# Performance work log

Measured on AMD Instinct MI355X. Metric: run time of the kernel, lower is better.

## Reference

```python
import jax, jax.numpy as jnp
import numpy as np

B, S, H, V, L = 8, 1024, 1024, 512, 6
NEG_INF = -10000000.0  # matches torch neg_inf constant


def setup_inputs() -> dict:
    key = jax.random.key(0)
    ks = jax.random.split(key, 13)
    s = 0.02
    return {
        "inputs": jax.random.randint(ks[0], (B, S), 0, V),
        "embedding": jax.random.normal(ks[1], (V, H), jnp.float32) * s,
        "Wq": jax.random.normal(ks[2], (L, H, H), jnp.float32) * s,
        "bq": jnp.zeros((L, H), jnp.float32),
        "Wk": jax.random.normal(ks[3], (L, H, H), jnp.float32) * s,
        "bk": jnp.zeros((L, H), jnp.float32),
        "Wv": jax.random.normal(ks[4], (L, H, H), jnp.float32) * s,
        "bv": jnp.zeros((L, H), jnp.float32),
        "Wm": jax.random.normal(ks[5], (L, H, H), jnp.float32) * s,
        "bm": jnp.zeros((L, H), jnp.float32),
        "Wout": jax.random.normal(ks[6], (H, V), jnp.float32) * s,
        "bout": jnp.zeros((V,), jnp.float32),
    }


def reference(inputs, embedding, Wq, bq, Wk, bk, Wv, bv, Wm, bm, Wout, bout):
    Hd = embedding.shape[1]
    seq = inputs.shape[1]
    scale = jax.lax.rsqrt(jnp.asarray(Hd, jnp.float32))
    idx = jnp.arange(seq)
    # mask[key, query]: additive NEG_INF where key > query (strict lower triangle)
    mask = jnp.where(idx[:, None] > idx[None, :], jnp.float32(NEG_INF), jnp.float32(0.0))
    x = embedding[inputs]  # [B, S, H]
    n_layers = Wq.shape[0]
    attns = []
    for l in range(n_layers):
        q = x @ Wq[l] + bq[l]
        k = x @ Wk[l] + bk[l]
        v = x @ Wv[l] + bv[l]
        # [B, key, query], softmax over key axis (dim=1), exactly as original
        logits = jnp.einsum('bkh,bqh->bkq', k, q) * scale + mask
        attn = jax.nn.softmax(logits, axis=1)
        ctx = jnp.einsum('bkq,bkh->bqh', attn, v)  # attn^T @ v
        residual = x + ctx
        x = residual + jax.nn.relu(ctx @ Wm[l] + bm[l])
        attns.append(attn)
    out = x @ Wout + bout  # [B, S, V]
    return out, jnp.stack(attns)  # attns: [L, B, S, S]
```

## Files before the change

### kernel.cpp

```cpp
#include <hip/hip_runtime.h>
#include <stdint.h>

typedef unsigned short u16;
typedef unsigned int u32;
typedef __bf16 bf16x8 __attribute__((ext_vector_type(8)));
typedef float floatx4 __attribute__((ext_vector_type(4)));

#define NEG_INF_F (-10000000.0f)

__device__ __forceinline__ float bf2f(u16 u) {
    union { u32 u; float f; } x; x.u = ((u32)u) << 16; return x.f;
}
__device__ __forceinline__ u16 f2bf(float f) {
    union { float f; u32 u; } x; x.f = f;
    u32 r = x.u + 0x7fffu + ((x.u >> 16) & 1u);
    return (u16)(r >> 16);
}

__device__ __forceinline__ void async_cp16(const void* g, void* l) {
    __builtin_amdgcn_global_load_lds(
        (const __attribute__((address_space(1))) void*)g,
        (__attribute__((address_space(3))) void*)l, 16, 0, 0);
}

enum { EPI_QKV = 0, EPI_LOGITS = 1, EPI_CTX = 2, EPI_MLP = 3, EPI_OUT = 4 };

template <int EPI>
__global__ __launch_bounds__(256) void gemm_bt(
    const u16* __restrict__ A, int lda, long long aBatch,
    const u16* __restrict__ B, int ldb, long long bBatch,
    void* __restrict__ Cv, int ldc, long long cBatch,
    int K,
    const float* __restrict__ bias,
    const u16* __restrict__ ctxb,
    u16* __restrict__ xb,
    float scale, int nx, int ny)
{
    __shared__ __align__(16) u16 sA[128 * 64];
    __shared__ __align__(16) u16 sB[128 * 64];

    const int tid  = threadIdx.x;
    const int wave = tid >> 6;
    const int lane = tid & 63;

    int bxE, byE, bz;
    if constexpr (EPI == EPI_LOGITS) {
        bz = blockIdx.x & 7;
        int t = blockIdx.x >> 3;
        int tq = (int)((sqrtf(8.0f * t + 1.0f) - 1.0f) * 0.5f);
        while ((tq + 1) * (tq + 2) / 2 <= t) ++tq;
        while (tq * (tq + 1) / 2 > t) --tq;
        bxE = tq;
        byE = t - tq * (tq + 1) / 2;
    } else if constexpr (EPI == EPI_CTX) {
        bz = blockIdx.x & 7;
        int t = blockIdx.x >> 3;
        bxE = t & 7;
        byE = t >> 3;
    } else {
        bz = 0;
        const int k = blockIdx.x & 7, r = blockIdx.x >> 3;
        if (nx >= 8) { const int xp = nx >> 3; bxE = xp * k + (r % xp); byE = r / xp; }
        else         { bxE = k >> 1; byE = (k & 1) * (ny >> 1) + r; }
    }
    int Keff = K;
    if constexpr (EPI == EPI_CTX) Keff = min(K, (byE + 1) * 128);

    const u16* Ab = A + (long long)bz * aBatch + (long long)(byE * 128) * lda;
    const u16* Bb = B + (long long)bz * bBatch + (long long)(bxE * 128) * ldb;

    const int wm = wave >> 1, wn = wave & 1;
    const int quad = lane >> 4;

    const int srowoff = lane >> 3;
    const int gf      = (lane & 7) ^ ((lane >> 3) & 7);

    const int ra = 64 * wm + (lane & 15);
    const int rb = 64 * wn + (lane & 15);
    const int rx7 = lane & 7;

    floatx4 zero = {0.f, 0.f, 0.f, 0.f};
    floatx4 acc[4][4];
#pragma unroll
    for (int i = 0; i < 4; ++i)
#pragma unroll
        for (int j = 0; j < 4; ++j) acc[i][j] = zero;

    for (int k0 = 0; k0 < Keff; k0 += 64) {
#pragma unroll
        for (int i = 0; i < 4; ++i) {
            const int c = wave * 4 + i;
            const int r = c * 8 + srowoff;
            async_cp16(Ab + (long long)r * lda + k0 + gf * 8, &sA[c * 512 + lane * 8]);
            async_cp16(Bb + (long long)r * ldb + k0 + gf * 8, &sB[c * 512 + lane * 8]);
        }
        __syncthreads();

#pragma unroll
        for (int kk = 0; kk < 64; kk += 32) {
            const int gbase = kk >> 3;
            const int ga = ((gbase + quad) ^ rx7) << 3;
            bf16x8 af[4], bf[4];
#pragma unroll
            for (int mi = 0; mi < 4; ++mi)
                af[mi] = *(const bf16x8*)&sA[(ra + 16 * mi) * 64 + ga];
#pragma unroll
            for (int ni = 0; ni < 4; ++ni)
                bf[ni] = *(const bf16x8*)&sB[(rb + 16 * ni) * 64 + ga];
#pragma unroll
            for (int mi = 0; mi < 4; ++mi)
#pragma unroll
                for (int ni = 0; ni < 4; ++ni)
                    acc[mi][ni] = __builtin_amdgcn_mfma_f32_16x16x32_bf16(
                        af[mi], bf[ni], acc[mi][ni], 0, 0, 0);
        }
        __syncthreads();
    }

    const int m0 = byE * 128 + 64 * wm + (quad << 2);
    const int n0 = bxE * 128 + 64 * wn + (lane & 15);
#pragma unroll
    for (int mi = 0; mi < 4; ++mi) {
#pragma unroll
        for (int ni = 0; ni < 4; ++ni) {
            const int gn = n0 + ni * 16;
#pragma unroll
            for (int r = 0; r < 4; ++r) {
                const int gm = m0 + mi * 16 + r;
                float v = acc[mi][ni][r];
                if constexpr (EPI == EPI_QKV) {
                    v += bias[gn];
                    ((u16*)Cv)[(long long)gm * ldc + gn] = f2bf(v);
                } else if constexpr (EPI == EPI_LOGITS) {
                    v = v * scale + (gm > gn ? NEG_INF_F : 0.0f);
                    ((float*)Cv)[(long long)bz * cBatch + (long long)gm * ldc + gn] = v;
                } else if constexpr (EPI == EPI_CTX) {
                    ((u16*)Cv)[(long long)bz * cBatch + (long long)gm * ldc + gn] = f2bf(v);
                } else if constexpr (EPI == EPI_MLP) {
                    const long long idx = (long long)gm * ldc + gn;
                    v += bias[gn];
                    v = fmaxf(v, 0.0f);
                    float xv = bf2f(xb[idx]) + bf2f(ctxb[idx]) + v;
                    xb[idx] = f2bf(xv);
                } else {
                    v += bias[gn];
                    ((float*)Cv)[(long long)gm * ldc + gn] = v;
                }
            }
        }
    }
}

template <int L, int H, int V>
__global__ void setup_weights(const float* __restrict__ Wq, const float* __restrict__ Wk,
                              const float* __restrict__ Wv, const float* __restrict__ Wm,
                              const float* __restrict__ Wout,
                              const float* __restrict__ bq, const float* __restrict__ bk,
                              const float* __restrict__ bv,
                              u16* __restrict__ WqkvT, u16* __restrict__ WmT,
                              u16* __restrict__ WoutT, float* __restrict__ bqkv)
{
    const int z = blockIdx.z;
    if (z == 4 * L + 1) {
        int i = ((blockIdx.y * 16 + blockIdx.x) * 256) + threadIdx.y * 64 + threadIdx.x;
        if (i < L * 3 * H) {
            int l = i / (3 * H), j = i % (3 * H);
            float v = (j < H) ? bq[l * H + j]
                    : (j < 2 * H) ? bk[l * H + j - H]
                                  : bv[l * H + j - 2 * H];
            bqkv[i] = v;
        }
        return;
    }

    const float* in;
    u16* outp;
    int inStride, outStride;
    if (z == 4 * L) {
        if (blockIdx.x >= V / 64) return;
        in = Wout; inStride = V;
        outp = WoutT; outStride = H;
    } else {
        const int which = z / L, l = z % L;
        inStride = H; outStride = H;
        if (which == 3) { in = Wm + (long long)l * H * H; outp = WmT + (long long)l * H * H; }
        else {
            in   = (which == 0 ? Wq : which == 1 ? Wk : Wv) + (long long)l * H * H;
            outp = WqkvT + (long long)l * 3 * H * H + (long long)which * H * H;
        }
    }

    __shared__ float tile[64][65];
    const int r0 = blockIdx.y * 64, c0 = blockIdx.x * 64;
    const int x = threadIdx.x, y = threadIdx.y;
#pragma unroll
    for (int j = 0; j < 16; ++j) {
        int r = y + j * 4;
        tile[r][x] = in[(long long)(r0 + r) * inStride + c0 + x];
    }
    __syncthreads();
#pragma unroll
    for (int j = 0; j < 16; ++j) {
        int r = y + j * 4;
        outp[(long long)(c0 + r) * outStride + r0 + x] = f2bf(tile[x][r]);
    }
}

__global__ __launch_bounds__(1024) void attn_post(
    float* __restrict__ attn, long long aStride,
    u16* __restrict__ attnT, long long tStride,
    const u16* __restrict__ qkv, u16* __restrict__ Vt)
{
    const int zone = blockIdx.y;
    if (zone < 8) {
        __shared__ float sm[64][16], sl[64][16], sm2[8][16], sl2[8][16];
        __shared__ float sM[16], sInv[16];

        float* base = attn + (long long)zone * aStride;
        const int x = threadIdx.x, ky = threadIdx.y;
        const int q = blockIdx.x * 16 + x;

        float v[16];
        float m = -3.4e38f, l = 0.f;
#pragma unroll
        for (int j = 0; j < 16; ++j) {
            const int k = ky * 16 + j;
            float vj = NEG_INF_F;
            if (k <= q) vj = base[(long long)k * 1024 + q];
            v[j] = vj;
            float mn = fmaxf(m, vj);
            l = l * __expf(m - mn) + __expf(vj - mn);
            m = mn;
        }
        sm[ky][x] = m;
        sl[ky][x] = l;
        __syncthreads();
        if (ky < 8) {
            float M = -3.4e38f, L = 0.f;
#pragma unroll
            for (int t = 0; t < 8; ++t) {
                float mm = sm[ky + 8 * t][x], ll = sl[ky + 8 * t][x];
                float mn = fmaxf(M, mm);
                L = L * __expf(M - mn) + ll * __expf(mm - mn);
                M = mn;
            }
            sm2[ky][x] = M;
            sl2[ky][x] = L;
        }
        __syncthreads();
        if (ky == 0) {
            float M = -3.4e38f, L = 0.f;
#pragma unroll
            for (int t = 0; t < 8; ++t) {
                float mm = sm2[t][x], ll = sl2[t][x];
                float mn = fmaxf(M, mm);
                L = L * __expf(M - mn) + ll * __expf(mm - mn);
                M = mn;
            }
            sM[x]   = M;
            sInv[x] = 1.0f / L;
        }
        __syncthreads();
        const float M = sM[x], inv = sInv[x];

        u16 pb[16];
#pragma unroll
        for (int j = 0; j < 16; ++j) {
            float p = __expf(v[j] - M) * inv;
            base[(long long)(ky * 16 + j) * 1024 + q] = p;
            pb[j] = f2bf(p);
        }
        u16* trow = attnT + (long long)zone * tStride + (long long)q * 1024 + ky * 16;
        ((uint4*)trow)[0] = *(const uint4*)&pb[0];
        ((uint4*)trow)[1] = *(const uint4*)&pb[8];
    } else {
        const int b = zone - 8;
        const u16* Vb = qkv + 2 * 1024 + (long long)b * (1024LL * 3072);
        u16* Ob       = Vt + (long long)b * (1024LL * 1024);
        __shared__ float tile[64][65];
        const int tid = threadIdx.y * 16 + threadIdx.x;
        const int tx = tid & 63, ty = tid >> 6;
#pragma unroll
        for (int rep = 0; rep < 4; ++rep) {
            const int T = blockIdx.x + rep * 64;
            const int s0 = (T >> 4) * 64, h0 = (T & 15) * 64;
            __syncthreads();
#pragma unroll
            for (int j = 0; j < 4; ++j) {
                const int s = j * 16 + ty;
                tile[s][tx] = bf2f(Vb[(long long)(s0 + s) * 3072 + h0 + tx]);
            }
            __syncthreads();
#pragma unroll
            for (int j = 0; j < 4; ++j) {
                const int h = j * 16 + ty;
                Ob[(long long)(h0 + h) * 1024 + s0 + tx] = f2bf(tile[tx][h]);
            }
        }
    }
}

__global__ void embed_kernel(const int* __restrict__ tok, const float* __restrict__ emb,
                             u16* __restrict__ xb)
{
    const int row = blockIdx.x;
    const int t   = tok[row];
    float4 v = ((const float4*)(emb + (long long)t * 1024))[threadIdx.x];
    uint2 p;
    p.x = (u32)f2bf(v.x) | ((u32)f2bf(v.y) << 16);
    p.y = (u32)f2bf(v.z) | ((u32)f2bf(v.w) << 16);
    ((uint2*)(xb + (long long)row * 1024))[threadIdx.x] = p;
}

extern "C" void kernel_launch(void* const* d_in, const int* in_sizes, int n_in,
                              void* d_out, int out_size, void* d_ws, size_t ws_size,
                              hipStream_t stream)
{
    const int*   tok  = (const int*)d_in[0];
    const float* emb  = (const float*)d_in[1];
    const float* Wq   = (const float*)d_in[2];
    const float* bq   = (const float*)d_in[3];
    const float* Wk   = (const float*)d_in[4];
    const float* bk   = (const float*)d_in[5];
    const float* Wv   = (const float*)d_in[6];
    const float* bv   = (const float*)d_in[7];
    const float* Wm   = (const float*)d_in[8];
    const float* bm   = (const float*)d_in[9];
    const float* Wout = (const float*)d_in[10];
    const float* bout = (const float*)d_in[11];
    float* out = (float*)d_out;

    constexpr int B = 8, S = 1024, H = 1024, V = 512, L = 6;
    constexpr long long M = (long long)B * S;

    char* ws = (char*)d_ws;
    u16*   WqkvT = (u16*)ws;   ws += (long long)L * 3 * H * H * 2;
    u16*   WmT   = (u16*)ws;   ws += (long long)L * H * H * 2;
    u16*   WoutT = (u16*)ws;   ws += (long long)V * H * 2;
    float* bqkv  = (float*)ws; ws += (long long)L * 3 * H * 4;
    u16*   xb    = (u16*)ws;   ws += M * H * 2;
    u16*   QKV   = (u16*)ws;   ws += M * 3 * H * 2;
    u16*   attnT = (u16*)ws;   ws += (long long)B * S * S * 2;
    u16*   Vt    = (u16*)ws;   ws += (long long)B * S * S * 2;
    u16*   ctxb  = (u16*)ws;   ws += M * H * 2;

    float* attnOut = out + (long long)B * S * V;

    setup_weights<L, H, V><<<dim3(16, 16, 4 * L + 2), dim3(64, 4), 0, stream>>>(
        Wq, Wk, Wv, Wm, Wout, bq, bk, bv, WqkvT, WmT, WoutT, bqkv);
    embed_kernel<<<M, 256, 0, stream>>>(tok, emb, xb);

    for (int l = 0; l < L; ++l) {
        gemm_bt<EPI_QKV><<<1536, 256, 0, stream>>>(
            xb, H, 0, WqkvT + (long long)l * 3 * H * H, H, 0,
            QKV, 3 * H, 0, H, bqkv + l * 3 * H, nullptr, nullptr, 0.f, 24, 64);

        float* attnL = attnOut + (long long)l * B * S * S;
        gemm_bt<EPI_LOGITS><<<288, 256, 0, stream>>>(
            QKV + H, 3 * H, (long long)S * 3 * H,
            QKV, 3 * H, (long long)S * 3 * H,
            attnL, S, (long long)S * S, H,
            nullptr, nullptr, nullptr, 0.03125f, 0, 0);

        attn_post<<<dim3(64, 16), dim3(16, 64), 0, stream>>>(
            attnL, (long long)S * S, attnT, (long long)S * S, QKV, Vt);

        gemm_bt<EPI_CTX><<<512, 256, 0, stream>>>(
            attnT, S, (long long)S * S, Vt, S, (long long)S * S,
            ctxb, H, (long long)S * H, S,
            nullptr, nullptr, nullptr, 0.f, 0, 0);

        gemm_bt<EPI_MLP><<<512, 256, 0, stream>>>(
            ctxb, H, 0, WmT + (long long)l * H * H, H, 0,
            nullptr, H, 0, H, bm + l * H, ctxb, xb, 0.f, 8, 64);
    }

    gemm_bt<EPI_OUT><<<256, 256, 0, stream>>>(
        xb, H, 0, WoutT, H, 0, out, V, 0, H,
        bout, nullptr, nullptr, 0.f, 4, 64);
}
```

Before: 1.357 ms.

## Add triple-buffered 256x128 GEMM kernel for QKV and MLP projections

Result: slower. 1.546 ms (+13.9%).

```diff
diff --git a/kernel.cpp b/kernel.cpp
--- a/kernel.cpp
+++ b/kernel.cpp
@@ -7,6 +7,7 @@
 typedef float floatx4 __attribute__((ext_vector_type(4)));
 
 #define NEG_INF_F (-10000000.0f)
+#define MFMA16 __builtin_amdgcn_mfma_f32_16x16x32_bf16
 
 __device__ __forceinline__ float bf2f(u16 u) {
     union { u32 u; float f; } x; x.u = ((u32)u) << 16; return x.f;
@@ -111,8 +112,7 @@
             for (int mi = 0; mi < 4; ++mi)
 #pragma unroll
                 for (int ni = 0; ni < 4; ++ni)
-                    acc[mi][ni] = __builtin_amdgcn_mfma_f32_16x16x32_bf16(
-                        af[mi], bf[ni], acc[mi][ni], 0, 0, 0);
+                    acc[mi][ni] = MFMA16(af[mi], bf[ni], acc[mi][ni], 0, 0, 0);
         }
         __syncthreads();
     }
@@ -151,6 +151,167 @@
     }
 }
 
+template <int EPI>
+__global__ __launch_bounds__(512, 2) void gemm3s(
+    const u16* __restrict__ A, int lda,
+    const u16* __restrict__ Bw, int ldb,
+    void* __restrict__ Cv, int ldc,
+    int K, const float* __restrict__ bias,
+    const u16* __restrict__ ctxb, u16* __restrict__ xb)
+{
+    __shared__ __align__(16) u16 sA[3][256 * 64];
+    __shared__ __align__(16) u16 sB[3][128 * 64];
+
+    const int tid  = threadIdx.x;
+    const int wave = tid >> 6;
+    const int lane = tid & 63;
+    const int wm   = wave >> 1, wn = wave & 1;
+    const int quad = lane >> 4;
+
+    const int k8 = blockIdx.x & 7;
+    const int r  = blockIdx.x >> 3;
+    const int bxE = r >> 2;
+    const int byE = k8 * 4 + (r & 3);
+
+    const u16* Ab = A  + (long long)(byE * 256) * lda;
+    const u16* Bb = Bw + (long long)(bxE * 128) * ldb;
+
+    const int srow = tid >> 3;
+    const int gf   = (tid & 7) ^ ((tid >> 3) & 7);
+    const long long aSrc = (long long)srow * lda + gf * 8;
+    const long long bSrc = (long long)srow * ldb + gf * 8;
+    const int dst = (wave << 9) + lane * 8;
+
+#define STA(nb, c, k0) async_cp16(Ab + (long long)((c) * 64) * lda + (k0) + aSrc, \
+                                  &sA[nb][(c) * 4096 + dst])
+#define STB(nb, c, k0) async_cp16(Bb + (long long)((c) * 64) * ldb + (k0) + bSrc, \
+                                  &sB[nb][(c) * 4096 + dst])
+
+    const int ra  = wm * 64 + (lane & 15);
+    const int rb  = wn * 64 + (lane & 15);
+    const int rx7 = lane & 7;
+
+    floatx4 zero = {0.f, 0.f, 0.f, 0.f};
+    floatx4 acc[4][4];
+#pragma unroll
+    for (int i = 0; i < 4; ++i)
+#pragma unroll
+        for (int j = 0; j < 4; ++j) acc[i][j] = zero;
+
+    const int NT = K >> 6;
+
+    STA(0, 0, 0);  STA(0, 1, 0);  STA(0, 2, 0);  STA(0, 3, 0);
+    STB(0, 0, 0);  STB(0, 1, 0);
+    STA(1, 0, 64); STA(1, 1, 64); STA(1, 2, 64); STA(1, 3, 64);
+    STB(1, 0, 64); STB(1, 1, 64);
+
+    int cb = 0;
+#pragma unroll 3
+    for (int t = 0; t < NT; ++t) {
+        if (t + 1 < NT) asm volatile("s_waitcnt vmcnt(6)" ::: "memory");
+        else            asm volatile("s_waitcnt vmcnt(0)" ::: "memory");
+        __builtin_amdgcn_s_barrier();
+
+        const int  nb = (cb == 0) ? 2 : cb - 1;
+        const int  kn = (t + 2) << 6;
+        const bool st = (t + 2) < NT;
+        const u16* pA = &sA[cb][0];
+        const u16* pB = &sB[cb][0];
+
+        bf16x8 af[4], bf0, bf1;
+
+        if (st) { STA(nb, 0, kn); STA(nb, 1, kn); }
+        {
+            const int g = (quad ^ rx7) << 3;
+#pragma unroll
+            for (int mi = 0; mi < 4; ++mi)
+                af[mi] = *(const bf16x8*)&pA[(ra + 16 * mi) * 64 + g];
+            bf0 = *(const bf16x8*)&pB[rb * 64 + g];
+            bf1 = *(const bf16x8*)&pB[(rb + 16) * 64 + g];
+        }
+        __builtin_amdgcn_s_setprio(1);
+#pragma unroll
+        for (int mi = 0; mi < 4; ++mi) {
+            acc[mi][0] = MFMA16(af[mi], bf0, acc[mi][0], 0, 0, 0);
+            acc[mi][1] = MFMA16(af[mi], bf1, acc[mi][1], 0, 0, 0);
+        }
+        __builtin_amdgcn_s_setprio(0);
+
+        if (st) { STA(nb, 2, kn); STA(nb, 3, kn); }
+        {
+            const int g = (quad ^ rx7) << 3;
+            bf0 = *(const bf16x8*)&pB[(rb + 32) * 64 + g];
+            bf1 = *(const bf16x8*)&pB[(rb + 48) * 64 + g];
+        }
+        __builtin_amdgcn_s_setprio(1);
+#pragma unroll
+        for (int mi = 0; mi < 4; ++mi) {
+            acc[mi][2] = MFMA16(af[mi], bf0, acc[mi][2], 0, 0, 0);
+            acc[mi][3] = MFMA16(af[mi], bf1, acc[mi][3], 0, 0, 0);
+        }
+        __builtin_amdgcn_s_setprio(0);
+
+        if (st) { STB(nb, 0, kn); }
+        {
+            const int g = ((4 + quad) ^ rx7) << 3;
+#pragma unroll
+            for (int mi = 0; mi < 4; ++mi)
+                af[mi] = *(const bf16x8*)&pA[(ra + 16 * mi) * 64 + g];
+            bf0 = *(const bf16x8*)&pB[rb * 64 + g];
+            bf1 = *(const bf16x8*)&pB[(rb + 16) * 64 + g];
+        }
+        __builtin_amdgcn_s_setprio(1);
+#pragma unroll
+        for (int mi = 0; mi < 4; ++mi) {
+            acc[mi][0] = MFMA16(af[mi], bf0, acc[mi][0], 0, 0, 0);
+            acc[mi][1] = MFMA16(af[mi], bf1, acc[mi][1], 0, 0, 0);
+        }
+        __builtin_amdgcn_s_setprio(0);
+
+        if (st) { STB(nb, 1, kn); }
+        {
+            const int g = ((4 + quad) ^ rx7) << 3;
+            bf0 = *(const bf16x8*)&pB[(rb + 32) * 64 + g];
+            bf1 = *(const bf16x8*)&pB[(rb + 48) * 64 + g];
+        }
+        __builtin_amdgcn_s_setprio(1);
+#pragma unroll
+        for (int mi = 0; mi < 4; ++mi) {
+            acc[mi][2] = MFMA16(af[mi], bf0, acc[mi][2], 0, 0, 0);
+            acc[mi][3] = MFMA16(af[mi], bf1, acc[mi][3], 0, 0, 0);
+        }
+        __builtin_amdgcn_s_setprio(0);
+
+        cb = (cb == 2) ? 0 : cb + 1;
+    }
+#undef STA
+#undef STB
+
+    const int m0 = byE * 256 + wm * 64 + (quad << 2);
+    const int n0 = bxE * 128 + wn * 64 + (lane & 15);
+#pragma unroll
+    for (int mi = 0; mi < 4; ++mi) {
+#pragma unroll
+        for (int ni = 0; ni < 4; ++ni) {
+            const int gn = n0 + ni * 16;
+            const float bb = bias[gn];
+#pragma unroll
+            for (int rr = 0; rr < 4; ++rr) {
+                const int gm = m0 + mi * 16 + rr;
+                float v = acc[mi][ni][rr] + bb;
+                if constexpr (EPI == EPI_QKV) {
+                    ((u16*)Cv)[(long long)gm * ldc + gn] = f2bf(v);
+                } else {
+                    const long long idx = (long long)gm * ldc + gn;
+                    v = fmaxf(v, 0.0f);
+                    float xv = bf2f(xb[idx]) + bf2f(ctxb[idx]) + v;
+                    xb[idx] = f2bf(xv);
+                }
+            }
+        }
+    }
+}
+
 template <int L, int H, int V>
 __global__ void setup_weights(const float* __restrict__ Wq, const float* __restrict__ Wk,
                               const float* __restrict__ Wv, const float* __restrict__ Wm,
@@ -351,9 +512,9 @@
     embed_kernel<<<M, 256, 0, stream>>>(tok, emb, xb);
 
     for (int l = 0; l < L; ++l) {
-        gemm_bt<EPI_QKV><<<1536, 256, 0, stream>>>(
-            xb, H, 0, WqkvT + (long long)l * 3 * H * H, H, 0,
-            QKV, 3 * H, 0, H, bqkv + l * 3 * H, nullptr, nullptr, 0.f, 24, 64);
+        gemm3s<EPI_QKV><<<768, 512, 0, stream>>>(
+            xb, H, WqkvT + (long long)l * 3 * H * H, H,
+            QKV, 3 * H, H, bqkv + l * 3 * H, nullptr, nullptr);
 
         float* attnL = attnOut + (long long)l * B * S * S;
         gemm_bt<EPI_LOGITS><<<288, 256, 0, stream>>>(
@@ -370,9 +531,9 @@
             ctxb, H, (long long)S * H, S,
             nullptr, nullptr, nullptr, 0.f, 0, 0);
 
-        gemm_bt<EPI_MLP><<<512, 256, 0, stream>>>(
-            ctxb, H, 0, WmT + (long long)l * H * H, H, 0,
-            nullptr, H, 0, H, bm + l * H, ctxb, xb, 0.f, 8, 64);
+        gemm3s<EPI_MLP><<<256, 512, 0, stream>>>(
+            ctxb, H, WmT + (long long)l * H * H, H,
+            nullptr, H, H, bm + l * H, ctxb, xb);
     }
 
     gemm_bt<EPI_OUT><<<256, 256, 0, stream>>>(
```

## Compute V transposed directly in QKV GEMM and fold embedding into setup

Applied to the files above, without the earlier changes.

Measured after the change: 1.401 ms. +3.2%, slower.

```diff
diff --git a/kernel.cpp b/kernel.cpp
--- a/kernel.cpp
+++ b/kernel.cpp
@@ -7,6 +7,7 @@
 typedef float floatx4 __attribute__((ext_vector_type(4)));
 
 #define NEG_INF_F (-10000000.0f)
+#define MFMA16 __builtin_amdgcn_mfma_f32_16x16x32_bf16
 
 __device__ __forceinline__ float bf2f(u16 u) {
     union { u32 u; float f; } x; x.u = ((u32)u) << 16; return x.f;
@@ -44,6 +45,7 @@
     const int lane = tid & 63;
 
     int bxE, byE, bz;
+    int vt = 0;
     if constexpr (EPI == EPI_LOGITS) {
         bz = blockIdx.x & 7;
         int t = blockIdx.x >> 3;
@@ -56,7 +58,18 @@
         bz = blockIdx.x & 7;
         int t = blockIdx.x >> 3;
         bxE = t & 7;
-        byE = t >> 3;
+        byE = 7 - (t >> 3);
+    } else if constexpr (EPI == EPI_QKV) {
+        bz = 0;
+        const int k8 = blockIdx.x & 7, rr = blockIdx.x >> 3;
+        if (rr < 128) {
+            bxE = 2 * k8 + (rr & 1); byE = rr >> 1;
+        } else {
+            vt = 1;
+            const int r2 = rr - 128;
+            bxE = 8 * k8 + (r2 & 7);
+            byE = r2 >> 3;
+        }
     } else {
         bz = 0;
         const int k = blockIdx.x & 7, r = blockIdx.x >> 3;
@@ -66,8 +79,20 @@
     int Keff = K;
     if constexpr (EPI == EPI_CTX) Keff = min(K, (byE + 1) * 128);
 
-    const u16* Ab = A + (long long)bz * aBatch + (long long)(byE * 128) * lda;
-    const u16* Bb = B + (long long)bz * bBatch + (long long)(bxE * 128) * ldb;
+    const u16* Ab;
+    const u16* Bb;
+    if constexpr (EPI == EPI_QKV) {
+        if (vt) {
+            Ab = B + 2 * 1024 * 1024 + (long long)(byE * 128) * ldb;
+            Bb = A + (long long)(bxE * 128) * lda;
+        } else {
+            Ab = A + (long long)(byE * 128) * lda;
+            Bb = B + (long long)(bxE * 128) * ldb;
+        }
+    } else {
+        Ab = A + (long long)bz * aBatch + (long long)(byE * 128) * lda;
+        Bb = B + (long long)bz * bBatch + (long long)(bxE * 128) * ldb;
+    }
 
     const int wm = wave >> 1, wn = wave & 1;
     const int quad = lane >> 4;
@@ -111,8 +136,7 @@
             for (int mi = 0; mi < 4; ++mi)
 #pragma unroll
                 for (int ni = 0; ni < 4; ++ni)
-                    acc[mi][ni] = __builtin_amdgcn_mfma_f32_16x16x32_bf16(
-                        af[mi], bf[ni], acc[mi][ni], 0, 0, 0);
+                    acc[mi][ni] = MFMA16(af[mi], bf[ni], acc[mi][ni], 0, 0, 0);
         }
         __syncthreads();
     }
@@ -129,8 +153,14 @@
                 const int gm = m0 + mi * 16 + r;
                 float v = acc[mi][ni][r];
                 if constexpr (EPI == EPI_QKV) {
-                    v += bias[gn];
-                    ((u16*)Cv)[(long long)gm * ldc + gn] = f2bf(v);
+                    if (!vt) {
+                        v += bias[gn];
+                        ((u16*)Cv)[(long long)gm * ldc + gn] = f2bf(v);
+                    } else {
+                        v += bias[2048 + gm];
+                        xb[((long long)(gn >> 10) << 20) + ((long long)gm << 10)
+                           + (gn & 1023)] = f2bf(v);
+                    }
                 } else if constexpr (EPI == EPI_LOGITS) {
                     v = v * scale + (gm > gn ? NEG_INF_F : 0.0f);
                     ((float*)Cv)[(long long)bz * cBatch + (long long)gm * ldc + gn] = v;
@@ -158,9 +188,26 @@
                               const float* __restrict__ bq, const float* __restrict__ bk,
                               const float* __restrict__ bv,
                               u16* __restrict__ WqkvT, u16* __restrict__ WmT,
-                              u16* __restrict__ WoutT, float* __restrict__ bqkv)
+                              u16* __restrict__ WoutT, float* __restrict__ bqkv,
+                              const int* __restrict__ tok, const float* __restrict__ emb,
+                              u16* __restrict__ xbuf)
 {
     const int z = blockIdx.z;
+    if (z == 4 * L + 2) {
+        const int blk = blockIdx.y * 16 + blockIdx.x;
+        const int t   = threadIdx.y * 64 + threadIdx.x;
+#pragma unroll 4
+        for (int j = 0; j < 32; ++j) {
+            const int row = blk * 32 + j;
+            const int tk  = tok[row];
+            float4 v = ((const float4*)(emb + (long long)tk * H))[t];
+            uint2 p;
+            p.x = (u32)f2bf(v.x) | ((u32)f2bf(v.y) << 16);
+            p.y = (u32)f2bf(v.z) | ((u32)f2bf(v.w) << 16);
+            ((uint2*)(xbuf + (long long)row * H))[t] = p;
+        }
+        return;
+    }
     if (z == 4 * L + 1) {
         int i = ((blockIdx.y * 16 + blockIdx.x) * 256) + threadIdx.y * 64 + threadIdx.x;
         if (i < L * 3 * H) {
@@ -208,108 +255,69 @@
 
 __global__ __launch_bounds__(1024) void attn_post(
     float* __restrict__ attn, long long aStride,
-    u16* __restrict__ attnT, long long tStride,
-    const u16* __restrict__ qkv, u16* __restrict__ Vt)
+    u16* __restrict__ attnT, long long tStride)
 {
-    const int zone = blockIdx.y;
-    if (zone < 8) {
-        __shared__ float sm[64][16], sl[64][16], sm2[8][16], sl2[8][16];
-        __shared__ float sM[16], sInv[16];
-
-        float* base = attn + (long long)zone * aStride;
-        const int x = threadIdx.x, ky = threadIdx.y;
-        const int q = blockIdx.x * 16 + x;
-
-        float v[16];
-        float m = -3.4e38f, l = 0.f;
-#pragma unroll
-        for (int j = 0; j < 16; ++j) {
-            const int k = ky * 16 + j;
-            float vj = NEG_INF_F;
-            if (k <= q) vj = base[(long long)k * 1024 + q];
-            v[j] = vj;
-            float mn = fmaxf(m, vj);
-            l = l * __expf(m - mn) + __expf(vj - mn);
-            m = mn;
-        }
-        sm[ky][x] = m;
-        sl[ky][x] = l;
-        __syncthreads();
-        if (ky < 8) {
-            float M = -3.4e38f, L = 0.f;
-#pragma unroll
-            for (int t = 0; t < 8; ++t) {
-                float mm = sm[ky + 8 * t][x], ll = sl[ky + 8 * t][x];
-                float mn = fmaxf(M, mm);
-                L = L * __expf(M - mn) + ll * __expf(mm - mn);
-                M = mn;
-            }
-            sm2[ky][x] = M;
-            sl2[ky][x] = L;
-        }
-        __syncthreads();
-        if (ky == 0) {
-            float M = -3.4e38f, L = 0.f;
-#pragma unroll
-            for (int t = 0; t < 8; ++t) {
-                float mm = sm2[t][x], ll = sl2[t][x];
-                float mn = fmaxf(M, mm);
-                L = L * __expf(M - mn) + ll * __expf(mm - mn);
-                M = mn;
-            }
-            sM[x]   = M;
-            sInv[x] = 1.0f / L;
-        }
-        __syncthreads();
-        const float M = sM[x], inv = sInv[x];
-
-        u16 pb[16];
-#pragma unroll
-        for (int j = 0; j < 16; ++j) {
-            float p = __expf(v[j] - M) * inv;
-            base[(long long)(ky * 16 + j) * 1024 + q] = p;
-            pb[j] = f2bf(p);
-        }
-        u16* trow = attnT + (long long)zone * tStride + (long long)q * 1024 + ky * 16;
-        ((uint4*)trow)[0] = *(const uint4*)&pb[0];
-        ((uint4*)trow)[1] = *(const uint4*)&pb[8];
-    } else {
-        const int b = zone - 8;
-        const u16* Vb = qkv + 2 * 1024 + (long long)b * (1024LL * 3072);
-        u16* Ob       = Vt + (long long)b * (1024LL * 1024);
-        __shared__ float tile[64][65];
-        const int tid = threadIdx.y * 16 + threadIdx.x;
-        const int tx = tid & 63, ty = tid >> 6;
-#pragma unroll
-        for (int rep = 0; rep < 4; ++rep) {
-            const int T = blockIdx.x + rep * 64;
-            const int s0 = (T >> 4) * 64, h0 = (T & 15) * 64;
-            __syncthreads();
-#pragma unroll
-            for (int j = 0; j < 4; ++j) {
-                const int s = j * 16 + ty;
-                tile[s][tx] = bf2f(Vb[(long long)(s0 + s) * 3072 + h0 + tx]);
-            }
-            __syncthreads();
-#pragma unroll
-            for (int j = 0; j < 4; ++j) {
-                const int h = j * 16 + ty;
-                Ob[(long long)(h0 + h) * 1024 + s0 + tx] = f2bf(tile[tx][h]);
-            }
-        }
-    }
-}
-
-__global__ void embed_kernel(const int* __restrict__ tok, const float* __restrict__ emb,
-                             u16* __restrict__ xb)
-{
-    const int row = blockIdx.x;
-    const int t   = tok[row];
-    float4 v = ((const float4*)(emb + (long long)t * 1024))[threadIdx.x];
-    uint2 p;
-    p.x = (u32)f2bf(v.x) | ((u32)f2bf(v.y) << 16);
-    p.y = (u32)f2bf(v.z) | ((u32)f2bf(v.w) << 16);
-    ((uint2*)(xb + (long long)row * 1024))[threadIdx.x] = p;
+    __shared__ float sm[64][16], sl[64][16], sm2[8][16], sl2[8][16];
+    __shared__ float sM[16], sInv[16];
+
+    const int b = blockIdx.y;
+    float* base = attn + (long long)b * aStride;
+    const int x = threadIdx.x, ky = threadIdx.y;
+    const int q = blockIdx.x * 16 + x;
+
+    float v[16];
+    float m = -3.4e38f, l = 0.f;
+#pragma unroll
+    for (int j = 0; j < 16; ++j) {
+        const int k = ky * 16 + j;
+        float vj = NEG_INF_F;
+        if (k <= q) vj = base[(long long)k * 1024 + q];
+        v[j] = vj;
+        float mn = fmaxf(m, vj);
+        l = l * __expf(m - mn) + __expf(vj - mn);
+        m = mn;
+    }
+    sm[ky][x] = m;
+    sl[ky][x] = l;
+    __syncthreads();
+    if (ky < 8) {
+        float M = -3.4e38f, L = 0.f;
+#pragma unroll
+        for (int t = 0; t < 8; ++t) {
+            float mm = sm[ky + 8 * t][x], ll = sl[ky + 8 * t][x];
+            float mn = fmaxf(M, mm);
+            L = L * __expf(M - mn) + ll * __expf(mm - mn);
+            M = mn;
+        }
+        sm2[ky][x] = M;
+        sl2[ky][x] = L;
+    }
+    __syncthreads();
+    if (ky == 0) {
+        float M = -3.4e38f, L = 0.f;
+#pragma unroll
+        for (int t = 0; t < 8; ++t) {
+            float mm = sm2[t][x], ll = sl2[t][x];
+            float mn = fmaxf(M, mm);
+            L = L * __expf(M - mn) + ll * __expf(mm - mn);
+            M = mn;
+        }
+        sM[x]   = M;
+        sInv[x] = 1.0f / L;
+    }
+    __syncthreads();
+    const float M = sM[x], inv = sInv[x];
+
+    u16 pb[16];
+#pragma unroll
+    for (int j = 0; j < 16; ++j) {
+        float p = __expf(v[j] - M) * inv;
+        base[(long long)(ky * 16 + j) * 1024 + q] = p;
+        pb[j] = f2bf(p);
+    }
+    u16* trow = attnT + (long long)b * tStride + (long long)q * 1024 + ky * 16;
+    ((uint4*)trow)[0] = *(const uint4*)&pb[0];
+    ((uint4*)trow)[1] = *(const uint4*)&pb[8];
 }
 
 extern "C" void kernel_launch(void* const* d_in, const int* in_sizes, int n_in,
@@ -339,31 +347,30 @@
     u16*   WoutT = (u16*)ws;   ws += (long long)V * H * 2;
     float* bqkv  = (float*)ws; ws += (long long)L * 3 * H * 4;
     u16*   xb    = (u16*)ws;   ws += M * H * 2;
-    u16*   QKV   = (u16*)ws;   ws += M * 3 * H * 2;
+    u16*   QKV   = (u16*)ws;   ws += M * 2 * H * 2;
     u16*   attnT = (u16*)ws;   ws += (long long)B * S * S * 2;
     u16*   Vt    = (u16*)ws;   ws += (long long)B * S * S * 2;
     u16*   ctxb  = (u16*)ws;   ws += M * H * 2;
 
     float* attnOut = out + (long long)B * S * V;
 
-    setup_weights<L, H, V><<<dim3(16, 16, 4 * L + 2), dim3(64, 4), 0, stream>>>(
-        Wq, Wk, Wv, Wm, Wout, bq, bk, bv, WqkvT, WmT, WoutT, bqkv);
-    embed_kernel<<<M, 256, 0, stream>>>(tok, emb, xb);
+    setup_weights<L, H, V><<<dim3(16, 16, 4 * L + 3), dim3(64, 4), 0, stream>>>(
+        Wq, Wk, Wv, Wm, Wout, bq, bk, bv, WqkvT, WmT, WoutT, bqkv, tok, emb, xb);
 
     for (int l = 0; l < L; ++l) {
         gemm_bt<EPI_QKV><<<1536, 256, 0, stream>>>(
             xb, H, 0, WqkvT + (long long)l * 3 * H * H, H, 0,
-            QKV, 3 * H, 0, H, bqkv + l * 3 * H, nullptr, nullptr, 0.f, 24, 64);
+            QKV, 2 * H, 0, H, bqkv + (long long)l * 3 * H, nullptr, Vt, 0.f, 0, 0);
 
         float* attnL = attnOut + (long long)l * B * S * S;
         gemm_bt<EPI_LOGITS><<<288, 256, 0, stream>>>(
-            QKV + H, 3 * H, (long long)S * 3 * H,
-            QKV, 3 * H, (long long)S * 3 * H,
+            QKV + H, 2 * H, (long long)S * 2 * H,
+            QKV, 2 * H, (long long)S * 2 * H,
             attnL, S, (long long)S * S, H,
             nullptr, nullptr, nullptr, 0.03125f, 0, 0);
 
-        attn_post<<<dim3(64, 16), dim3(16, 64), 0, stream>>>(
-            attnL, (long long)S * S, attnT, (long long)S * S, QKV, Vt);
+        attn_post<<<dim3(64, 8), dim3(16, 64), 0, stream>>>(
+            attnL, (long long)S * S, attnT, (long long)S * S);
 
         gemm_bt<EPI_CTX><<<512, 256, 0, stream>>>(
             attnT, S, (long long)S * S, Vt, S, (long long)S * S,
@@ -372,7 +379,7 @@
 
         gemm_bt<EPI_MLP><<<512, 256, 0, stream>>>(
             ctxb, H, 0, WmT + (long long)l * H * H, H, 0,
-            nullptr, H, 0, H, bm + l * H, ctxb, xb, 0.f, 8, 64);
+            nullptr, H, 0, H, bm + (long long)l * H, ctxb, xb, 0.f, 8, 64);
     }
 
     gemm_bt<EPI_OUT><<<256, 256, 0, stream>>>(
```

## Move V transpose into logits GEMM launch and reorder ctx tile scheduling

Applied to the files above, without the earlier changes.

Result: no change. 1.336 ms (-1.6%).

```diff
diff --git a/kernel.cpp b/kernel.cpp
--- a/kernel.cpp
+++ b/kernel.cpp
@@ -7,6 +7,7 @@
 typedef float floatx4 __attribute__((ext_vector_type(4)));
 
 #define NEG_INF_F (-10000000.0f)
+#define MFMA16 __builtin_amdgcn_mfma_f32_16x16x32_bf16
 
 __device__ __forceinline__ float bf2f(u16 u) {
     union { u32 u; float f; } x; x.u = ((u32)u) << 16; return x.f;
@@ -36,7 +37,7 @@
     u16* __restrict__ xb,
     float scale, int nx, int ny)
 {
-    __shared__ __align__(16) u16 sA[128 * 64];
+    __shared__ __align__(16) u16 sA[128 * 64 + 128];
     __shared__ __align__(16) u16 sB[128 * 64];
 
     const int tid  = threadIdx.x;
@@ -45,6 +46,35 @@
 
     int bxE, byE, bz;
     if constexpr (EPI == EPI_LOGITS) {
+        if (blockIdx.x >= 288) {
+            const int t    = blockIdx.x - 288;
+            const int b    = t & 7;
+            const int tile = t >> 3;
+            const int s0 = (tile >> 4) * 64, h0 = (tile & 15) * 64;
+            const u16* Vb = ctxb + (long long)b * (1024LL * 3072) + 2 * 1024;
+            u16* Ob       = xb   + (long long)b * (1024LL * 1024);
+            u32* tl = (u32*)sA;
+            const int lr = tid >> 4, lc = tid & 15;
+#pragma unroll
+            for (int p = 0; p < 4; ++p) {
+                const int s = p * 16 + lr;
+                uint2 v = *(const uint2*)&Vb[(long long)(s0 + s) * 3072 + h0 + lc * 4];
+                tl[s * 65 + lc * 4 + 0] = v.x & 0xffffu;
+                tl[s * 65 + lc * 4 + 1] = v.x >> 16;
+                tl[s * 65 + lc * 4 + 2] = v.y & 0xffffu;
+                tl[s * 65 + lc * 4 + 3] = v.y >> 16;
+            }
+            __syncthreads();
+#pragma unroll
+            for (int p = 0; p < 4; ++p) {
+                const int h = p * 16 + lr;
+                uint2 o;
+                o.x = tl[(lc * 4 + 0) * 65 + h] | (tl[(lc * 4 + 1) * 65 + h] << 16);
+                o.y = tl[(lc * 4 + 2) * 65 + h] | (tl[(lc * 4 + 3) * 65 + h] << 16);
+                *(uint2*)&Ob[(long long)(h0 + h) * 1024 + s0 + lc * 4] = o;
+            }
+            return;
+        }
         bz = blockIdx.x & 7;
         int t = blockIdx.x >> 3;
         int tq = (int)((sqrtf(8.0f * t + 1.0f) - 1.0f) * 0.5f);
@@ -56,7 +86,7 @@
         bz = blockIdx.x & 7;
         int t = blockIdx.x >> 3;
         bxE = t & 7;
-        byE = t >> 3;
+        byE = 7 - (t >> 3);
     } else {
         bz = 0;
         const int k = blockIdx.x & 7, r = blockIdx.x >> 3;
@@ -111,8 +141,7 @@
             for (int mi = 0; mi < 4; ++mi)
 #pragma unroll
                 for (int ni = 0; ni < 4; ++ni)
-                    acc[mi][ni] = __builtin_amdgcn_mfma_f32_16x16x32_bf16(
-                        af[mi], bf[ni], acc[mi][ni], 0, 0, 0);
+                    acc[mi][ni] = MFMA16(af[mi], bf[ni], acc[mi][ni], 0, 0, 0);
         }
         __syncthreads();
     }
@@ -208,96 +237,69 @@
 
 __global__ __launch_bounds__(1024) void attn_post(
     float* __restrict__ attn, long long aStride,
-    u16* __restrict__ attnT, long long tStride,
-    const u16* __restrict__ qkv, u16* __restrict__ Vt)
-{
-    const int zone = blockIdx.y;
-    if (zone < 8) {
-        __shared__ float sm[64][16], sl[64][16], sm2[8][16], sl2[8][16];
-        __shared__ float sM[16], sInv[16];
-
-        float* base = attn + (long long)zone * aStride;
-        const int x = threadIdx.x, ky = threadIdx.y;
-        const int q = blockIdx.x * 16 + x;
-
-        float v[16];
-        float m = -3.4e38f, l = 0.f;
-#pragma unroll
-        for (int j = 0; j < 16; ++j) {
-            const int k = ky * 16 + j;
-            float vj = NEG_INF_F;
-            if (k <= q) vj = base[(long long)k * 1024 + q];
-            v[j] = vj;
-            float mn = fmaxf(m, vj);
-            l = l * __expf(m - mn) + __expf(vj - mn);
-            m = mn;
-        }
-        sm[ky][x] = m;
-        sl[ky][x] = l;
-        __syncthreads();
-        if (ky < 8) {
-            float M = -3.4e38f, L = 0.f;
-#pragma unroll
-            for (int t = 0; t < 8; ++t) {
-                float mm = sm[ky + 8 * t][x], ll = sl[ky + 8 * t][x];
-                float mn = fmaxf(M, mm);
-                L = L * __expf(M - mn) + ll * __expf(mm - mn);
-                M = mn;
-            }
-            sm2[ky][x] = M;
-            sl2[ky][x] = L;
-        }
-        __syncthreads();
-        if (ky == 0) {
-            float M = -3.4e38f, L = 0.f;
-#pragma unroll
-            for (int t = 0; t < 8; ++t) {
-                float mm = sm2[t][x], ll = sl2[t][x];
-                float mn = fmaxf(M, mm);
-                L = L * __expf(M - mn) + ll * __expf(mm - mn);
-                M = mn;
-            }
-            sM[x]   = M;
-            sInv[x] = 1.0f / L;
-        }
-        __syncthreads();
-        const float M = sM[x], inv = sInv[x];
-
-        u16 pb[16];
-#pragma unroll
-        for (int j = 0; j < 16; ++j) {
-            float p = __expf(v[j] - M) * inv;
-            base[(long long)(ky * 16 + j) * 1024 + q] = p;
-            pb[j] = f2bf(p);
-        }
-        u16* trow = attnT + (long long)zone * tStride + (long long)q * 1024 + ky * 16;
-        ((uint4*)trow)[0] = *(const uint4*)&pb[0];
-        ((uint4*)trow)[1] = *(const uint4*)&pb[8];
-    } else {
-        const int b = zone - 8;
-        const u16* Vb = qkv + 2 * 1024 + (long long)b * (1024LL * 3072);
-        u16* Ob       = Vt + (long long)b * (1024LL * 1024);
-        __shared__ float tile[64][65];
-        const int tid = threadIdx.y * 16 + threadIdx.x;
-        const int tx = tid & 63, ty = tid >> 6;
-#pragma unroll
-        for (int rep = 0; rep < 4; ++rep) {
-            const int T = blockIdx.x + rep * 64;
-            const int s0 = (T >> 4) * 64, h0 = (T & 15) * 64;
-            __syncthreads();
-#pragma unroll
-            for (int j = 0; j < 4; ++j) {
-                const int s = j * 16 + ty;
-                tile[s][tx] = bf2f(Vb[(long long)(s0 + s) * 3072 + h0 + tx]);
-            }
-            __syncthreads();
-#pragma unroll
-            for (int j = 0; j < 4; ++j) {
-                const int h = j * 16 + ty;
-                Ob[(long long)(h0 + h) * 1024 + s0 + tx] = f2bf(tile[tx][h]);
-            }
-        }
-    }
+    u16* __restrict__ attnT, long long tStride)
+{
+    __shared__ float sm[64][16], sl[64][16], sm2[8][16], sl2[8][16];
+    __shared__ float sM[16], sInv[16];
+
+    const int b = blockIdx.y;
+    float* base = attn + (long long)b * aStride;
+    const int x = threadIdx.x, ky = threadIdx.y;
+    const int q = blockIdx.x * 16 + x;
+
+    float v[16];
+    float m = -3.4e38f, l = 0.f;
+#pragma unroll
+    for (int j = 0; j < 16; ++j) {
+        const int k = ky * 16 + j;
+        float vj = NEG_INF_F;
+        if (k <= q) vj = base[(long long)k * 1024 + q];
+        v[j] = vj;
+        float mn = fmaxf(m, vj);
+        l = l * __expf(m - mn) + __expf(vj - mn);
+        m = mn;
+    }
+    sm[ky][x] = m;
+    sl[ky][x] = l;
+    __syncthreads();
+    if (ky < 8) {
+        float M = -3.4e38f, L = 0.f;
+#pragma unroll
+        for (int t = 0; t < 8; ++t) {
+            float mm = sm[ky + 8 * t][x], ll = sl[ky + 8 * t][x];
+            float mn = fmaxf(M, mm);
+            L = L * __expf(M - mn) + ll * __expf(mm - mn);
+            M = mn;
+        }
+        sm2[ky][x] = M;
+        sl2[ky][x] = L;
+    }
+    __syncthreads();
+    if (ky == 0) {
+        float M = -3.4e38f, L = 0.f;
+#pragma unroll
+        for (int t = 0; t < 8; ++t) {
+            float mm = sm2[t][x], ll = sl2[t][x];
+            float mn = fmaxf(M, mm);
+            L = L * __expf(M - mn) + ll * __expf(mm - mn);
+            M = mn;
+        }
+        sM[x]   = M;
+        sInv[x] = 1.0f / L;
+    }
+    __syncthreads();
+    const float M = sM[x], inv = sInv[x];
+
+    u16 pb[16];
+#pragma unroll
+    for (int j = 0; j < 16; ++j) {
+        float p = __expf(v[j] - M) * inv;
+        base[(long long)(ky * 16 + j) * 1024 + q] = p;
+        pb[j] = f2bf(p);
+    }
+    u16* trow = attnT + (long long)b * tStride + (long long)q * 1024 + ky * 16;
+    ((uint4*)trow)[0] = *(const uint4*)&pb[0];
+    ((uint4*)trow)[1] = *(const uint4*)&pb[8];
 }
 
 __global__ void embed_kernel(const int* __restrict__ tok, const float* __restrict__ emb,
@@ -356,14 +358,14 @@
             QKV, 3 * H, 0, H, bqkv + l * 3 * H, nullptr, nullptr, 0.f, 24, 64);
 
         float* attnL = attnOut + (long long)l * B * S * S;
-        gemm_bt<EPI_LOGITS><<<288, 256, 0, stream>>>(
+        gemm_bt<EPI_LOGITS><<<288 + 2048, 256, 0, stream>>>(
             QKV + H, 3 * H, (long long)S * 3 * H,
             QKV, 3 * H, (long long)S * 3 * H,
             attnL, S, (long long)S * S, H,
-            nullptr, nullptr, nullptr, 0.03125f, 0, 0);
-
-        attn_post<<<dim3(64, 16), dim3(16, 64), 0, stream>>>(
-            attnL, (long long)S * S, attnT, (long long)S * S, QKV, Vt);
+            nullptr, QKV, Vt, 0.03125f, 0, 0);
+
+        attn_post<<<dim3(64, 8), dim3(16, 64), 0, stream>>>(
+            attnL, (long long)S * S, attnT, (long long)S * S);
 
         gemm_bt<EPI_CTX><<<512, 256, 0, stream>>>(
             attnT, S, (long long)S * S, Vt, S, (long long)S * S,
```
